# Kernel tuning notes

Measured on AMD Instinct MI355X. Metric: run time of the kernel, lower is better.

## Reference

```python
import jax, jax.numpy as jnp
import numpy as np

WORLD_SIZE = 8  # number of ring participants / sequence blocks
NEG_INF = jnp.float32(-jnp.inf)


def setup_inputs() -> dict:
    key = jax.random.key(0)
    kq, kk, kv = jax.random.split(key, 3)
    B, S, H, D = 2, 8192, 16, 64
    return {
        "query": jax.random.normal(kq, (B, S, H, D), dtype=jnp.float32),
        "key": jax.random.normal(kk, (B, S, H, D), dtype=jnp.float32),
        "value": jax.random.normal(kv, (B, S, H, D), dtype=jnp.float32),
    }


def reference(query, key, value):
    """Ring attention: blockwise QK^T + per-block softmax with running
    (max, sum, acc) online-softmax merge across ring steps. Causal.
    query/key/value: [B, S, H, D]. Output: [B, S, H, D].
    Mathematically equal to exact causal attention, computed with the
    block/LSE-merge structure of the ring algorithm (never materializes
    the full [S, S] score matrix).
    """
    W = WORLD_SIZE
    B, S, H, D = query.shape
    Bs = S // W  # local block (per-rank) sequence length
    scale = 1.0 / np.sqrt(D)

    # [W, B, Bs, H, D] blocks along the sequence axis
    qb = query.reshape(B, W, Bs, H, D).transpose(1, 0, 2, 3, 4)
    kb = key.reshape(B, W, Bs, H, D).transpose(1, 0, 2, 3, 4)
    vb = value.reshape(B, W, Bs, H, D).transpose(1, 0, 2, 3, 4)

    diag_mask = jnp.arange(Bs)[:, None] >= jnp.arange(Bs)[None, :]  # [Bs, Bs]

    outs = []
    for r in range(W):  # query block owned by rank r
        q = qb[r]  # [B, Bs, H, D]
        m = jnp.full((B, H, Bs), NEG_INF, dtype=jnp.float32)   # running row max
        l = jnp.zeros((B, H, Bs), dtype=jnp.float32)           # running sum-exp
        acc = jnp.zeros((B, H, Bs, D), dtype=jnp.float32)      # running numerator
        for j in range(r + 1):  # causal: fully-masked future kv blocks skipped
            s = jnp.einsum('bqhd,bkhd->bhqk', q, kb[j]).astype(jnp.float32) * scale
            if j == r:  # diagonal block: per-element causal mask
                s = jnp.where(diag_mask, s, NEG_INF)
            m_new = jnp.maximum(m, s.max(axis=-1))
            p = jnp.exp(s - m_new[..., None])                   # [B, H, Bs, Bs]
            alpha = jnp.exp(m - m_new)
            l = l * alpha + p.sum(axis=-1)
            acc = acc * alpha[..., None] + jnp.einsum(
                'bhqk,bkhd->bhqd', p, vb[j].astype(jnp.float32))
            m = m_new
        out_r = (acc / l[..., None]).astype(query.dtype)  # [B, H, Bs, D]
        outs.append(out_r.transpose(0, 2, 1, 3))          # -> [B, Bs, H, D]
    return jnp.concatenate(outs, axis=1)  # [B, S, H, D]
```

## Files before the change

kernel.cpp:

```cpp
#include <hip/hip_runtime.h>
#include <hip/hip_bf16.h>

typedef __attribute__((ext_vector_type(8))) short short8;
typedef __attribute__((ext_vector_type(4))) short short4_t;
typedef __attribute__((ext_vector_type(2))) float float2_t;
typedef __attribute__((ext_vector_type(4))) float float4_t;
typedef __attribute__((ext_vector_type(16))) float floatx16;

constexpr int S_LEN = 8192;
constexpr int NHEAD = 16;
constexpr int DHEAD = 64;
constexpr int RS    = NHEAD * DHEAD;
constexpr int BK    = 64;
constexpr int QW    = 32;
constexpr int NWAVE = 8;
constexpr int QTILE = QW * NWAVE;
constexpr int BH    = 32;
constexpr int PADK  = 72;

constexpr size_t KB_ELEMS  = (size_t)BH * S_LEN * DHEAD;
constexpr size_t WS_NEEDED = 2 * KB_ELEMS * sizeof(unsigned short);

__device__ __forceinline__ unsigned int cvt2bf(float lo, float hi) {
  __hip_bfloat162 h2 = __float22bfloat162_rn(make_float2(lo, hi));
  unsigned int u;
  __builtin_memcpy(&u, &h2, 4);
  return u;
}

__device__ __forceinline__ float fast_exp2(float x) {
#if __has_builtin(__builtin_amdgcn_exp2f)
  return __builtin_amdgcn_exp2f(x);
#else
  return exp2f(x);
#endif
}

__device__ __forceinline__ void gload_lds16(const unsigned short* g, unsigned short* l) {
  __builtin_amdgcn_global_load_lds(
      (const __attribute__((address_space(1))) unsigned int*)g,
      (__attribute__((address_space(3))) unsigned int*)l, 16, 0, 0);
}

__global__ __launch_bounds__(256)
void prep_kernel(const float* __restrict__ Kg, const float* __restrict__ Vg,
                 unsigned short* __restrict__ Kb, unsigned short* __restrict__ Vb)
{
  const int t = threadIdx.x;
  if (blockIdx.x < 16384) {
    const int bs = blockIdx.x;
    const int b  = bs >> 13;
    const int s  = bs & 8191;
    const int hh = t >> 4;
    const int q4 = t & 15;

    const float* src = Kg + ((size_t)(b * S_LEN + s) * NHEAD + hh) * DHEAD + 4 * q4;
    float4_t v = *(const float4_t*)src;
    uint2 pk = make_uint2(cvt2bf(v[0], v[1]), cvt2bf(v[2], v[3]));

    const int slot = (q4 >> 1) ^ (s & 7);
    const int half = q4 & 1;
    unsigned short* dst = Kb + ((size_t)((b * NHEAD + hh) * S_LEN + s)) * DHEAD
                             + slot * 8 + half * 4;
    *(uint2*)dst = pk;
  } else {
    __shared__ float Lf[64 * 65];

    const int blk  = blockIdx.x - 16384;
    const int bh   = blk & 31;
    const int tile = blk >> 5;
    const int b    = bh >> 4;
    const int hh   = bh & 15;
    const int s0   = tile * 64;

    const int kvr = t >> 4;
    const int d4  = (t & 15) * 4;
#pragma unroll
    for (int p = 0; p < 4; ++p) {
      int kv = kvr + 16 * p;
      float4_t x = *(const float4_t*)&Vg[((size_t)(b * S_LEN + s0 + kv) * NHEAD + hh) * DHEAD + d4];
#pragma unroll
      for (int j = 0; j < 4; ++j) Lf[(d4 + j) * 65 + kv] = x[j];
    }
    __syncthreads();

    const int d2 = t >> 3;
    const int sp = t & 7;
#pragma unroll
    for (int i = 0; i < 2; ++i) {
      int dd    = d2 + 32 * i;
      int s_log = sp ^ (dd & 7);
      int kb    = 16 * (s_log >> 1) + 4 * (s_log & 1);
      const float* r = &Lf[dd * 65];
      uint4 pk = make_uint4(cvt2bf(r[kb + 0], r[kb + 1]),
                            cvt2bf(r[kb + 2], r[kb + 3]),
                            cvt2bf(r[kb + 8], r[kb + 9]),
                            cvt2bf(r[kb + 10], r[kb + 11]));
      *(uint4*)&Vb[(((size_t)(bh * 128 + tile)) * 64 + dd) * 64 + sp * 8] = pk;
    }
  }
}

__global__ __launch_bounds__(512, 4)
void fattn_fast(const float* __restrict__ Qg,
                const unsigned short* __restrict__ Kb,
                const unsigned short* __restrict__ Vb,
                float* __restrict__ Og)
{
  __shared__ __align__(16) unsigned short SM[2][2][4096];
  const unsigned short* SMf = &SM[0][0][0];

  const int tid  = threadIdx.x;
  const int wave = tid >> 6;
  const int lane = tid & 63;
  const int m31  = lane & 31;
  const int h    = lane >> 5;

  const int blk = blockIdx.x;
  const int bh  = blk & 31;
  const int qt  = 31 - (blk >> 5);
  const int b   = bh >> 4;
  const int h_  = bh & 15;

  const int q0  = qt * QTILE;
  const int qw0 = q0 + wave * QW;

  const size_t base = ((size_t)b * S_LEN * NHEAD + h_) * DHEAD;
  const float* Qp = Qg + base;
  float*       Op = Og + base;

  const unsigned short* kgp = Kb + (size_t)bh * (S_LEN * DHEAD) + wave * 512 + lane * 8;
  const unsigned short* vgp = Vb + (size_t)bh * (S_LEN * DHEAD) + wave * 512 + lane * 8;

  const float qs = 0.125f * 1.44269504088896340736f;
  short8 qf[4];
#pragma unroll
  for (int c = 0; c < 4; ++c) {
    const float* p = Qp + (size_t)(qw0 + m31) * RS + 16 * c + 8 * h;
    float4_t a = *(const float4_t*)p;
    float4_t d = *(const float4_t*)(p + 4);
    union { short8 s; unsigned int u[4]; } r;
    r.u[0] = cvt2bf(a[0] * qs, a[1] * qs);
    r.u[1] = cvt2bf(a[2] * qs, a[3] * qs);
    r.u[2] = cvt2bf(d[0] * qs, d[1] * qs);
    r.u[3] = cvt2bf(d[2] * qs, d[3] * qs);
    qf[c] = r.s;
  }

  floatx16 acc[2];
#pragma unroll
  for (int md = 0; md < 2; ++md)
#pragma unroll
    for (int r = 0; r < 16; ++r) acc[md][r] = 0.f;

  float l_run = 0.f;

  const int s7 = m31 & 7;
  int offK[2][4];
#pragma unroll
  for (int x = 0; x < 2; ++x)
#pragma unroll
    for (int c = 0; c < 4; ++c)
      offK[x][c] = (32 * x + m31) * 64 + (((2 * c + h) ^ s7) << 3);

  const int kend = q0 + QTILE;

  gload_lds16(kgp, &SM[0][0][wave * 512]);
  gload_lds16(vgp, &SM[0][1][wave * 512]);

  int cur = 0;
  for (int k0 = 0; k0 < kend; k0 += BK) {
    asm volatile("s_waitcnt vmcnt(0)" ::: "memory");
    __syncthreads();

    if (k0 + BK < kend) {
      const int nb = cur ^ 1;
      gload_lds16(kgp + (size_t)(k0 + BK) * 64, &SM[nb][0][wave * 512]);
      gload_lds16(vgp + (size_t)(k0 + BK) * 64, &SM[nb][1][wave * 512]);
    }

    if (k0 < qw0 + QW) {
      floatx16 ST[2];
      __builtin_amdgcn_s_setprio(1);
#pragma unroll
      for (int kvm2 = 0; kvm2 < 2; ++kvm2) {
#pragma unroll
        for (int r = 0; r < 16; ++r) ST[kvm2][r] = 0.f;
#pragma unroll
        for (int c = 0; c < 4; ++c) {
          short8 aK = *(const short8*)&SMf[offK[kvm2][c]];
          ST[kvm2] = __builtin_amdgcn_mfma_f32_32x32x16_bf16(aK, qf[c], ST[kvm2], 0, 0, 0);
        }
      }
      __builtin_amdgcn_s_setprio(0);

      if (k0 + BK > qw0) {
        const int qpos = qw0 + m31;
#pragma unroll
        for (int kvm2 = 0; kvm2 < 2; ++kvm2)
#pragma unroll
          for (int r = 0; r < 16; ++r) {
            int kpos = k0 + 32 * kvm2 + (r & 3) + 8 * (r >> 2) + 4 * h;
            if (kpos > qpos) ST[kvm2][r] = -__builtin_inff();
          }
      }

      unsigned int D[2][8];
      float2_t ps2 = {0.f, 0.f};
#pragma unroll
      for (int kvm2 = 0; kvm2 < 2; ++kvm2)
#pragma unroll
        for (int i = 0; i < 8; ++i) {
          float e0 = fast_exp2(ST[kvm2][2 * i]);
          float e1 = fast_exp2(ST[kvm2][2 * i + 1]);
          D[kvm2][i] = cvt2bf(e0, e1);
          float2_t e2 = {e0, e1};
          ps2 += e2;
        }
      l_run += ps2[0] + ps2[1];

      __builtin_amdgcn_s_setprio(1);
#pragma unroll
      for (int t = 0; t < 4; ++t) {
        const int u = t & 1;
        union { short8 s; unsigned int u32[4]; } bf;
        bf.u32[0] = D[t >> 1][4 * u + 0];
        bf.u32[1] = D[t >> 1][4 * u + 1];
        bf.u32[2] = D[t >> 1][4 * u + 2];
        bf.u32[3] = D[t >> 1][4 * u + 3];
#pragma unroll
        for (int md = 0; md < 2; ++md) {
          short8 aV = *(const short8*)&SMf[offK[md][t] + 4096];
          acc[md] = __builtin_amdgcn_mfma_f32_32x32x16_bf16(aV, bf.s, acc[md], 0, 0, 0);
        }
      }
      __builtin_amdgcn_s_setprio(0);
    }

#pragma unroll
    for (int x = 0; x < 2; ++x)
#pragma unroll
      for (int c = 0; c < 4; ++c) offK[x][c] ^= 8192;
    cur ^= 1;
  }

  float l = l_run + __shfl_xor(l_run, 32);
  float inv = 1.0f / l;
  float* op = Op + (size_t)(qw0 + m31) * RS;
#pragma unroll
  for (int md = 0; md < 2; ++md)
#pragma unroll
    for (int g = 0; g < 4; ++g) {
      float4_t o;
#pragma unroll
      for (int j = 0; j < 4; ++j) o[j] = acc[md][4 * g + j] * inv;
      *(float4_t*)(op + 32 * md + 8 * g + 4 * h) = o;
    }
}

__global__ __launch_bounds__(256, 4)
void fattn_legacy(const float* __restrict__ Qg,
                  const float* __restrict__ Kg,
                  const float* __restrict__ Vg,
                  float* __restrict__ Og)
{
  __shared__ __align__(16) unsigned short Kl[BK * PADK];
  __shared__ __align__(16) unsigned short Vl[DHEAD * PADK];

  const int tid  = threadIdx.x;
  const int wave = tid >> 6;
  const int lane = tid & 63;
  const int m31  = lane & 31;
  const int h    = lane >> 5;

  const int blk = blockIdx.x;
  const int bh  = blk & 31;
  const int qt  = 63 - (blk >> 5);
  const int b   = bh >> 4;
  const int h_  = bh & 15;

  const int q0  = qt * 128;
  const int qw0 = q0 + wave * QW;

  const size_t base = ((size_t)b * S_LEN * NHEAD + h_) * DHEAD;
  const float* Qp = Qg + base;
  const float* Kp = Kg + base;
  const float* Vp = Vg + base;
  float*       Op = Og + base;

  const float qs = 0.125f * 1.44269504088896340736f;
  short8 qf[4];
#pragma unroll
  for (int c = 0; c < 4; ++c) {
    const float* p = Qp + (size_t)(qw0 + m31) * RS + 16 * c + 8 * h;
    float4_t a = *(const float4_t*)p;
    float4_t d = *(const float4_t*)(p + 4);
    union { short8 s; unsigned int u[4]; } r;
    r.u[0] = cvt2bf(a[0] * qs, a[1] * qs);
    r.u[1] = cvt2bf(a[2] * qs, a[3] * qs);
    r.u[2] = cvt2bf(d[0] * qs, d[1] * qs);
    r.u[3] = cvt2bf(d[2] * qs, d[3] * qs);
    qf[c] = r.s;
  }

  floatx16 acc[2];
#pragma unroll
  for (int md = 0; md < 2; ++md)
#pragma unroll
    for (int r = 0; r < 16; ++r) acc[md][r] = 0.f;

  float l_run = 0.f;

  const int sr  = tid >> 4;
  const int sc4 = (tid & 15) * 4;
  const int vd  = tid & 63;
  const int vg0 = tid >> 6;

  const int kend = q0 + 128;
  for (int k0 = 0; k0 < kend; k0 += BK) {
    {
      const float* kp = Kp + (size_t)(k0 + sr) * RS + sc4;
#pragma unroll
      for (int ps = 0; ps < 4; ++ps) {
        float4_t v = *(const float4_t*)(kp + (size_t)ps * 16 * RS);
        uint2 pk = make_uint2(cvt2bf(v[0], v[1]), cvt2bf(v[2], v[3]));
        *(uint2*)&Kl[(sr + ps * 16) * PADK + sc4] = pk;
      }
#pragma unroll
      for (int p = 0; p < 2; ++p) {
        const int vg = vg0 + 4 * p;
        const float* vp = Vp + (size_t)(k0 + 8 * vg) * RS + vd;
        float x0 = vp[0 * RS], x1 = vp[1 * RS], x2 = vp[2 * RS], x3 = vp[3 * RS];
        float x4 = vp[4 * RS], x5 = vp[5 * RS], x6 = vp[6 * RS], x7 = vp[7 * RS];
        uint4 pk = make_uint4(cvt2bf(x0, x1), cvt2bf(x2, x3),
                              cvt2bf(x4, x5), cvt2bf(x6, x7));
        *(uint4*)&Vl[vd * PADK + 8 * vg] = pk;
      }
    }
    __syncthreads();

    if (k0 < qw0 + QW) {
      floatx16 ST[2];
#pragma unroll
      for (int kvm2 = 0; kvm2 < 2; ++kvm2) {
#pragma unroll
        for (int r = 0; r < 16; ++r) ST[kvm2][r] = 0.f;
#pragma unroll
        for (int c = 0; c < 4; ++c) {
          short8 aK = *(const short8*)&Kl[(32 * kvm2 + m31) * PADK + 16 * c + 8 * h];
          ST[kvm2] = __builtin_amdgcn_mfma_f32_32x32x16_bf16(aK, qf[c], ST[kvm2], 0, 0, 0);
        }
      }

      if (k0 + BK > qw0) {
        const int qpos = qw0 + m31;
#pragma unroll
        for (int kvm2 = 0; kvm2 < 2; ++kvm2)
#pragma unroll
          for (int r = 0; r < 16; ++r) {
            int kpos = k0 + 32 * kvm2 + (r & 3) + 8 * (r >> 2) + 4 * h;
            if (kpos > qpos) ST[kvm2][r] = -__builtin_inff();
          }
      }

      unsigned int D[2][8];
      float ps0 = 0.f, ps1 = 0.f;
#pragma unroll
      for (int kvm2 = 0; kvm2 < 2; ++kvm2)
#pragma unroll
        for (int i = 0; i < 8; ++i) {
          float e0 = fast_exp2(ST[kvm2][2 * i]);
          float e1 = fast_exp2(ST[kvm2][2 * i + 1]);
          D[kvm2][i] = cvt2bf(e0, e1);
          if (i & 1) ps1 += e0 + e1; else ps0 += e0 + e1;
        }
      l_run += ps0 + ps1;

#pragma unroll
      for (int t = 0; t < 4; ++t) {
        const int u  = t & 1;
        const int kb = 32 * (t >> 1) + 16 * u;
        union { short8 s; unsigned int u32[4]; } bf;
        bf.u32[0] = D[t >> 1][4 * u + 0];
        bf.u32[1] = D[t >> 1][4 * u + 1];
        bf.u32[2] = D[t >> 1][4 * u + 2];
        bf.u32[3] = D[t >> 1][4 * u + 3];
#pragma unroll
        for (int md = 0; md < 2; ++md) {
          const unsigned short* vr = &Vl[(32 * md + m31) * PADK + kb + 4 * h];
          short4_t lo = *(const short4_t*)(vr);
          short4_t hi = *(const short4_t*)(vr + 8);
          short8 aV = __builtin_shufflevector(lo, hi, 0, 1, 2, 3, 4, 5, 6, 7);
          acc[md] = __builtin_amdgcn_mfma_f32_32x32x16_bf16(aV, bf.s, acc[md], 0, 0, 0);
        }
      }
    }
    __syncthreads();
  }

  float l = l_run + __shfl_xor(l_run, 32);
  float inv = 1.0f / l;
  float* op = Op + (size_t)(qw0 + m31) * RS;
#pragma unroll
  for (int md = 0; md < 2; ++md)
#pragma unroll
    for (int g = 0; g < 4; ++g) {
      float4_t o;
#pragma unroll
      for (int j = 0; j < 4; ++j) o[j] = acc[md][4 * g + j] * inv;
      *(float4_t*)(op + 32 * md + 8 * g + 4 * h) = o;
    }
}

extern "C" void kernel_launch(void* const* d_in, const int* in_sizes, int n_in,
                              void* d_out, int out_size, void* d_ws, size_t ws_size,
                              hipStream_t stream) {
  const float* q = (const float*)d_in[0];
  const float* k = (const float*)d_in[1];
  const float* v = (const float*)d_in[2];
  float* o = (float*)d_out;

  if (d_ws != nullptr && ws_size >= WS_NEEDED) {
    unsigned short* Kb = (unsigned short*)d_ws;
    unsigned short* Vb = Kb + KB_ELEMS;
    prep_kernel<<<dim3(20480), dim3(256), 0, stream>>>(k, v, Kb, Vb);
    fattn_fast <<<dim3(1024),  dim3(512), 0, stream>>>(q, Kb, Vb, o);
  } else {
    fattn_legacy<<<dim3(2048), dim3(256), 0, stream>>>(q, k, v, o);
  }
}
```

Before: 506.1 us.

## Pair causal query tiles per block and read V fragments directly from global

The fast attention kernel now runs 4 waves with 128-row query tiles, and each block handles two tiles (qt and 63-qt) one after the other, so every block does about the same amount of causal work. Only K is staged through double-buffered LDS. V fragments are loaded straight from global/L2 into registers, and the setprio hints are removed. This is meant to fix load imbalance across the causal triangle and halve LDS traffic. The cost is latency-exposed global V loads in the inner loop and smaller workgroups.

Result: slower. 923.3 us (+82.4%).

```diff
diff --git a/kernel.cpp b/kernel.cpp
--- a/kernel.cpp
+++ b/kernel.cpp
@@ -3,7 +3,6 @@
 
 typedef __attribute__((ext_vector_type(8))) short short8;
 typedef __attribute__((ext_vector_type(4))) short short4_t;
-typedef __attribute__((ext_vector_type(2))) float float2_t;
 typedef __attribute__((ext_vector_type(4))) float float4_t;
 typedef __attribute__((ext_vector_type(16))) float floatx16;
 
@@ -13,7 +12,7 @@
 constexpr int RS    = NHEAD * DHEAD;
 constexpr int BK    = 64;
 constexpr int QW    = 32;
-constexpr int NWAVE = 8;
+constexpr int NWAVE = 4;
 constexpr int QTILE = QW * NWAVE;
 constexpr int BH    = 32;
 constexpr int PADK  = 72;
@@ -101,14 +100,13 @@
   }
 }
 
-__global__ __launch_bounds__(512, 4)
+__global__ __launch_bounds__(256, 4)
 void fattn_fast(const float* __restrict__ Qg,
                 const unsigned short* __restrict__ Kb,
                 const unsigned short* __restrict__ Vb,
                 float* __restrict__ Og)
 {
-  __shared__ __align__(16) unsigned short SM[2][2][4096];
-  const unsigned short* SMf = &SM[0][0][0];
+  __shared__ __align__(16) unsigned short SM[2][4096];
 
   const int tid  = threadIdx.x;
   const int wave = tid >> 6;
@@ -118,19 +116,177 @@
 
   const int blk = blockIdx.x;
   const int bh  = blk & 31;
-  const int qt  = 31 - (blk >> 5);
+  const int pr  = blk >> 5;
   const int b   = bh >> 4;
   const int h_  = bh & 15;
-
-  const int q0  = qt * QTILE;
-  const int qw0 = q0 + wave * QW;
 
   const size_t base = ((size_t)b * S_LEN * NHEAD + h_) * DHEAD;
   const float* Qp = Qg + base;
   float*       Op = Og + base;
 
-  const unsigned short* kgp = Kb + (size_t)bh * (S_LEN * DHEAD) + wave * 512 + lane * 8;
-  const unsigned short* vgp = Vb + (size_t)bh * (S_LEN * DHEAD) + wave * 512 + lane * 8;
+  const unsigned short* kbh = Kb + (size_t)bh * (S_LEN * DHEAD);
+  const unsigned short* vbh = Vb + (size_t)bh * (S_LEN * DHEAD);
+  const unsigned short* kgp = kbh + wave * 512 + lane * 8;
+
+  const int s7 = m31 & 7;
+  int off[2][4];
+#pragma unroll
+  for (int x = 0; x < 2; ++x)
+#pragma unroll
+    for (int c = 0; c < 4; ++c)
+      off[x][c] = (32 * x + m31) * 64 + (((2 * c + h) ^ s7) << 3);
+
+  const float qs = 0.125f * 1.44269504088896340736f;
+
+#pragma unroll 1
+  for (int seg = 0; seg < 2; ++seg) {
+    const int qt  = seg ? pr : (63 - pr);
+    const int q0  = qt * QTILE;
+    const int qw0 = q0 + wave * QW;
+
+    short8 qf[4];
+#pragma unroll
+    for (int c = 0; c < 4; ++c) {
+      const float* p = Qp + (size_t)(qw0 + m31) * RS + 16 * c + 8 * h;
+      float4_t a = *(const float4_t*)p;
+      float4_t d = *(const float4_t*)(p + 4);
+      union { short8 s; unsigned int u[4]; } r;
+      r.u[0] = cvt2bf(a[0] * qs, a[1] * qs);
+      r.u[1] = cvt2bf(a[2] * qs, a[3] * qs);
+      r.u[2] = cvt2bf(d[0] * qs, d[1] * qs);
+      r.u[3] = cvt2bf(d[2] * qs, d[3] * qs);
+      qf[c] = r.s;
+    }
+
+    floatx16 acc[2];
+#pragma unroll
+    for (int md = 0; md < 2; ++md)
+#pragma unroll
+      for (int r = 0; r < 16; ++r) acc[md][r] = 0.f;
+    float l_run = 0.f;
+
+    const int kend = q0 + QTILE;
+
+    gload_lds16(kgp,        &SM[0][wave * 512]);
+    gload_lds16(kgp + 2048, &SM[0][wave * 512 + 2048]);
+
+    int cur = 0;
+    for (int k0 = 0; k0 < kend; k0 += BK) {
+      asm volatile("s_waitcnt vmcnt(0)" ::: "memory");
+      __syncthreads();
+
+      if (k0 + BK < kend) {
+        const unsigned short* kp = kgp + (size_t)(k0 + BK) * 64;
+        const int nb = cur ^ 1;
+        gload_lds16(kp,        &SM[nb][wave * 512]);
+        gload_lds16(kp + 2048, &SM[nb][wave * 512 + 2048]);
+      }
+
+      if (k0 < qw0 + QW) {
+        floatx16 ST[2];
+#pragma unroll
+        for (int kvm2 = 0; kvm2 < 2; ++kvm2) {
+#pragma unroll
+          for (int r = 0; r < 16; ++r) ST[kvm2][r] = 0.f;
+#pragma unroll
+          for (int c = 0; c < 4; ++c) {
+            short8 aK = *(const short8*)&SM[cur][off[kvm2][c]];
+            ST[kvm2] = __builtin_amdgcn_mfma_f32_32x32x16_bf16(aK, qf[c], ST[kvm2], 0, 0, 0);
+          }
+        }
+
+        const unsigned short* vtile = vbh + (size_t)k0 * 64;
+        short8 vf[2][4];
+#pragma unroll
+        for (int md = 0; md < 2; ++md)
+#pragma unroll
+          for (int t = 0; t < 4; ++t)
+            vf[md][t] = *(const short8*)&vtile[off[md][t]];
+
+        if (k0 + BK > qw0) {
+          const int qpos = qw0 + m31;
+#pragma unroll
+          for (int kvm2 = 0; kvm2 < 2; ++kvm2)
+#pragma unroll
+            for (int r = 0; r < 16; ++r) {
+              int kpos = k0 + 32 * kvm2 + (r & 3) + 8 * (r >> 2) + 4 * h;
+              if (kpos > qpos) ST[kvm2][r] = -__builtin_inff();
+            }
+        }
+
+        unsigned int D[2][8];
+        float ps0 = 0.f, ps1 = 0.f;
+#pragma unroll
+        for (int kvm2 = 0; kvm2 < 2; ++kvm2)
+#pragma unroll
+          for (int i = 0; i < 8; ++i) {
+            float e0 = fast_exp2(ST[kvm2][2 * i]);
+            float e1 = fast_exp2(ST[kvm2][2 * i + 1]);
+            D[kvm2][i] = cvt2bf(e0, e1);
+            if (i & 1) ps1 += e0 + e1; else ps0 += e0 + e1;
+          }
+        l_run += ps0 + ps1;
+
+#pragma unroll
+        for (int t = 0; t < 4; ++t) {
+          const int u = t & 1;
+          union { short8 s; unsigned int u32[4]; } bf;
+          bf.u32[0] = D[t >> 1][4 * u + 0];
+          bf.u32[1] = D[t >> 1][4 * u + 1];
+          bf.u32[2] = D[t >> 1][4 * u + 2];
+          bf.u32[3] = D[t >> 1][4 * u + 3];
+#pragma unroll
+          for (int md = 0; md < 2; ++md)
+            acc[md] = __builtin_amdgcn_mfma_f32_32x32x16_bf16(vf[md][t], bf.s, acc[md], 0, 0, 0);
+        }
+      }
+      cur ^= 1;
+    }
+
+    float l = l_run + __shfl_xor(l_run, 32);
+    float inv = 1.0f / l;
+    float* op = Op + (size_t)(qw0 + m31) * RS;
+#pragma unroll
+    for (int md = 0; md < 2; ++md)
+#pragma unroll
+      for (int g = 0; g < 4; ++g) {
+        float4_t o;
+#pragma unroll
+        for (int j = 0; j < 4; ++j) o[j] = acc[md][4 * g + j] * inv;
+        *(float4_t*)(op + 32 * md + 8 * g + 4 * h) = o;
+      }
+  }
+}
+
+__global__ __launch_bounds__(256, 4)
+void fattn_legacy(const float* __restrict__ Qg,
+                  const float* __restrict__ Kg,
+                  const float* __restrict__ Vg,
+                  float* __restrict__ Og)
+{
+  __shared__ __align__(16) unsigned short Kl[BK * PADK];
+  __shared__ __align__(16) unsigned short Vl[DHEAD * PADK];
+
+  const int tid  = threadIdx.x;
+  const int wave = tid >> 6;
+  const int lane = tid & 63;
+  const int m31  = lane & 31;
+  const int h    = lane >> 5;
+
+  const int blk = blockIdx.x;
+  const int bh  = blk & 31;
+  const int qt  = 63 - (blk >> 5);
+  const int b   = bh >> 4;
+  const int h_  = bh & 15;
+
+  const int q0  = qt * 128;
+  const int qw0 = q0 + wave * 32;
+
+  const size_t base = ((size_t)b * S_LEN * NHEAD + h_) * DHEAD;
+  const float* Qp = Qg + base;
+  const float* Kp = Kg + base;
+  const float* Vp = Vg + base;
+  float*       Op = Og + base;
 
   const float qs = 0.125f * 1.44269504088896340736f;
   short8 qf[4];
@@ -155,162 +311,6 @@
 
   float l_run = 0.f;
 
-  const int s7 = m31 & 7;
-  int offK[2][4];
-#pragma unroll
-  for (int x = 0; x < 2; ++x)
-#pragma unroll
-    for (int c = 0; c < 4; ++c)
-      offK[x][c] = (32 * x + m31) * 64 + (((2 * c + h) ^ s7) << 3);
-
-  const int kend = q0 + QTILE;
-
-  gload_lds16(kgp, &SM[0][0][wave * 512]);
-  gload_lds16(vgp, &SM[0][1][wave * 512]);
-
-  int cur = 0;
-  for (int k0 = 0; k0 < kend; k0 += BK) {
-    asm volatile("s_waitcnt vmcnt(0)" ::: "memory");
-    __syncthreads();
-
-    if (k0 + BK < kend) {
-      const int nb = cur ^ 1;
-      gload_lds16(kgp + (size_t)(k0 + BK) * 64, &SM[nb][0][wave * 512]);
-      gload_lds16(vgp + (size_t)(k0 + BK) * 64, &SM[nb][1][wave * 512]);
-    }
-
-    if (k0 < qw0 + QW) {
-      floatx16 ST[2];
-      __builtin_amdgcn_s_setprio(1);
-#pragma unroll
-      for (int kvm2 = 0; kvm2 < 2; ++kvm2) {
-#pragma unroll
-        for (int r = 0; r < 16; ++r) ST[kvm2][r] = 0.f;
-#pragma unroll
-        for (int c = 0; c < 4; ++c) {
-          short8 aK = *(const short8*)&SMf[offK[kvm2][c]];
-          ST[kvm2] = __builtin_amdgcn_mfma_f32_32x32x16_bf16(aK, qf[c], ST[kvm2], 0, 0, 0);
-        }
-      }
-      __builtin_amdgcn_s_setprio(0);
-
-      if (k0 + BK > qw0) {
-        const int qpos = qw0 + m31;
-#pragma unroll
-        for (int kvm2 = 0; kvm2 < 2; ++kvm2)
-#pragma unroll
-          for (int r = 0; r < 16; ++r) {
-            int kpos = k0 + 32 * kvm2 + (r & 3) + 8 * (r >> 2) + 4 * h;
-            if (kpos > qpos) ST[kvm2][r] = -__builtin_inff();
-          }
-      }
-
-      unsigned int D[2][8];
-      float2_t ps2 = {0.f, 0.f};
-#pragma unroll
-      for (int kvm2 = 0; kvm2 < 2; ++kvm2)
-#pragma unroll
-        for (int i = 0; i < 8; ++i) {
-          float e0 = fast_exp2(ST[kvm2][2 * i]);
-          float e1 = fast_exp2(ST[kvm2][2 * i + 1]);
-          D[kvm2][i] = cvt2bf(e0, e1);
-          float2_t e2 = {e0, e1};
-          ps2 += e2;
-        }
-      l_run += ps2[0] + ps2[1];
-
-      __builtin_amdgcn_s_setprio(1);
-#pragma unroll
-      for (int t = 0; t < 4; ++t) {
-        const int u = t & 1;
-        union { short8 s; unsigned int u32[4]; } bf;
-        bf.u32[0] = D[t >> 1][4 * u + 0];
-        bf.u32[1] = D[t >> 1][4 * u + 1];
-        bf.u32[2] = D[t >> 1][4 * u + 2];
-        bf.u32[3] = D[t >> 1][4 * u + 3];
-#pragma unroll
-        for (int md = 0; md < 2; ++md) {
-          short8 aV = *(const short8*)&SMf[offK[md][t] + 4096];
-          acc[md] = __builtin_amdgcn_mfma_f32_32x32x16_bf16(aV, bf.s, acc[md], 0, 0, 0);
-        }
-      }
-      __builtin_amdgcn_s_setprio(0);
-    }
-
-#pragma unroll
-    for (int x = 0; x < 2; ++x)
-#pragma unroll
-      for (int c = 0; c < 4; ++c) offK[x][c] ^= 8192;
-    cur ^= 1;
-  }
-
-  float l = l_run + __shfl_xor(l_run, 32);
-  float inv = 1.0f / l;
-  float* op = Op + (size_t)(qw0 + m31) * RS;
-#pragma unroll
-  for (int md = 0; md < 2; ++md)
-#pragma unroll
-    for (int g = 0; g < 4; ++g) {
-      float4_t o;
-#pragma unroll
-      for (int j = 0; j < 4; ++j) o[j] = acc[md][4 * g + j] * inv;
-      *(float4_t*)(op + 32 * md + 8 * g + 4 * h) = o;
-    }
-}
-
-__global__ __launch_bounds__(256, 4)
-void fattn_legacy(const float* __restrict__ Qg,
-                  const float* __restrict__ Kg,
-                  const float* __restrict__ Vg,
-                  float* __restrict__ Og)
-{
-  __shared__ __align__(16) unsigned short Kl[BK * PADK];
-  __shared__ __align__(16) unsigned short Vl[DHEAD * PADK];
-
-  const int tid  = threadIdx.x;
-  const int wave = tid >> 6;
-  const int lane = tid & 63;
-  const int m31  = lane & 31;
-  const int h    = lane >> 5;
-
-  const int blk = blockIdx.x;
-  const int bh  = blk & 31;
-  const int qt  = 63 - (blk >> 5);
-  const int b   = bh >> 4;
-  const int h_  = bh & 15;
-
-  const int q0  = qt * 128;
-  const int qw0 = q0 + wave * QW;
-
-  const size_t base = ((size_t)b * S_LEN * NHEAD + h_) * DHEAD;
-  const float* Qp = Qg + base;
-  const float* Kp = Kg + base;
-  const float* Vp = Vg + base;
-  float*       Op = Og + base;
-
-  const float qs = 0.125f * 1.44269504088896340736f;
-  short8 qf[4];
-#pragma unroll
-  for (int c = 0; c < 4; ++c) {
-    const float* p = Qp + (size_t)(qw0 + m31) * RS + 16 * c + 8 * h;
-    float4_t a = *(const float4_t*)p;
-    float4_t d = *(const float4_t*)(p + 4);
-    union { short8 s; unsigned int u[4]; } r;
-    r.u[0] = cvt2bf(a[0] * qs, a[1] * qs);
-    r.u[1] = cvt2bf(a[2] * qs, a[3] * qs);
-    r.u[2] = cvt2bf(d[0] * qs, d[1] * qs);
-    r.u[3] = cvt2bf(d[2] * qs, d[3] * qs);
-    qf[c] = r.s;
-  }
-
-  floatx16 acc[2];
-#pragma unroll
-  for (int md = 0; md < 2; ++md)
-#pragma unroll
-    for (int r = 0; r < 16; ++r) acc[md][r] = 0.f;
-
-  float l_run = 0.f;
-
   const int sr  = tid >> 4;
   const int sc4 = (tid & 15) * 4;
   const int vd  = tid & 63;
@@ -339,7 +339,7 @@
     }
     __syncthreads();
 
-    if (k0 < qw0 + QW) {
+    if (k0 < qw0 + 32) {
       floatx16 ST[2];
 #pragma unroll
       for (int kvm2 = 0; kvm2 < 2; ++kvm2) {
@@ -424,7 +424,7 @@
     unsigned short* Kb = (unsigned short*)d_ws;
     unsigned short* Vb = Kb + KB_ELEMS;
     prep_kernel<<<dim3(20480), dim3(256), 0, stream>>>(k, v, Kb, Vb);
-    fattn_fast <<<dim3(1024),  dim3(512), 0, stream>>>(q, Kb, Vb, o);
+    fattn_fast <<<dim3(1024),  dim3(256), 0, stream>>>(q, Kb, Vb, o);
   } else {
     fattn_legacy<<<dim3(2048), dim3(256), 0, stream>>>(q, k, v, o);
   }
```
